# Optimization experiments

Hardware: AMD Instinct MI355X
Metric: run time of the kernel (lower is better)

## Reference

```python
import jax, jax.numpy as jnp
import numpy as np

N = 40962          # icosphere level-6 vertex count
E = 245772         # N * k (k=6 knn, directed)
MUL_IN = 8         # '8x0e + 8x1o' -> dim 8 + 24 = 32
MUL_OUT = 16       # '16x0e + 16x1o' -> dim 16 + 48 = 64
H = 64             # radial MLP hidden
WNUM = 4 * MUL_IN * MUL_OUT  # 512 per-edge TP weights (4 CG paths)
SQ3 = np.float32(np.sqrt(3.0))


def setup_inputs() -> dict:
    key = jax.random.key(0)
    ks = jax.random.split(key, 8)
    x = jax.random.normal(ks[0], (N, MUL_IN + 3 * MUL_IN), dtype=jnp.float32)
    pos = jax.random.normal(ks[1], (N, 3), dtype=jnp.float32)
    src = jax.random.randint(ks[2], (E,), 0, N)
    dst = jax.random.randint(ks[3], (E,), 0, N)
    edge_index = jnp.stack([src, dst]).astype(jnp.int32)
    W1 = jax.random.normal(ks[4], (1, H), dtype=jnp.float32)
    W2 = jax.random.normal(ks[5], (H, WNUM), dtype=jnp.float32)
    Ws = jax.random.normal(ks[6], (MUL_OUT, MUL_OUT), dtype=jnp.float32)
    k7, k8 = jax.random.split(ks[7])
    Wns = jax.random.normal(k7, (MUL_OUT, MUL_OUT), dtype=jnp.float32)
    Wg = jax.random.normal(k8, (MUL_OUT, MUL_OUT), dtype=jnp.float32)
    return {"x": x, "pos": pos, "edge_index": edge_index,
            "W1": W1, "W2": W2, "Ws": Ws, "Wns": Wns, "Wg": Wg}


def reference(x, pos, edge_index, W1, W2, Ws, Wns, Wg):
    src, dst = edge_index[0], edge_index[1]
    xs = x[:, :MUL_IN]                                  # (N, 8)  scalars (0e)
    xv = x[:, MUL_IN:].reshape(-1, MUL_IN, 3)           # (N, 8, 3) vectors (1o)

    # --- edge geometry + spherical harmonics (component-normalized, lmax=1) ---
    edge_vec = pos[dst] - pos[src]                      # (E, 3)
    edge_len = jnp.maximum(jnp.linalg.norm(edge_vec, axis=-1, keepdims=True), 1e-8)
    edge_dir = edge_vec / edge_len                      # (E, 3)
    Y1 = SQ3 * edge_dir                                 # l=1 SH; l=0 SH == 1

    # --- radial MLP -> per-edge tensor-product weights (shared_weights=False) ---
    h = jax.nn.silu(edge_len @ W1)                      # (E, H), fan_in = 1
    w = (h @ W2) * (1.0 / np.sqrt(np.float32(H)))       # (E, 512)
    wA, wB, wC, wD = [wi.reshape(-1, MUL_IN, MUL_OUT)
                      for wi in jnp.split(w, 4, axis=1)]

    xs_e = xs[src]                                      # (E, 8)   gather
    xv_e = xv[src]                                      # (E, 8, 3) gather
    norm = np.float32(1.0 / np.sqrt(2.0 * MUL_IN))      # path normalization

    # --- tensor product: 4 CG paths ---
    # 0e x 0e -> 0e  (CG = 1)
    pathA = jnp.einsum('eu,euw->ew', xs_e, wA)
    # 1o x 1o -> 0e  (CG_ij = delta_ij / sqrt(3))
    dot = jnp.einsum('eui,ei->eu', xv_e, Y1) * (1.0 / SQ3)
    pathB = jnp.einsum('eu,euw->ew', dot, wB)
    m_s = (pathA + pathB) * norm                        # (E, 16)
    # 0e x 1o -> 1o  (CG = identity)
    pathC = jnp.einsum('eu,euw->ew', xs_e, wC)[:, :, None] * Y1[:, None, :]
    # 1o x 0e -> 1o  (CG = identity)
    pathD = jnp.einsum('eui,euw->ewi', xv_e, wD)
    m_v = (pathC + pathD) * norm                        # (E, 16, 3)

    m = jnp.concatenate([m_s, m_v.reshape(-1, 3 * MUL_OUT)], axis=1)  # (E, 64)

    # --- scatter-add to destination nodes (index_add) ---
    out = jnp.zeros((x.shape[0], m.shape[1]), dtype=x.dtype).at[dst].add(m)

    # --- gated equivariant nonlinearity (o3.Linear with fan-in norm) ---
    lin_norm = np.float32(1.0 / np.sqrt(np.float32(MUL_OUT)))
    os_ = out[:, :MUL_OUT]                              # (N, 16)
    ov_ = out[:, MUL_OUT:].reshape(-1, MUL_OUT, 3)      # (N, 16, 3)
    s = jax.nn.silu(os_ @ Ws * lin_norm)                # (N, 16)
    ns = jnp.einsum('nui,uw->nwi', ov_, Wns) * lin_norm # (N, 16, 3)
    g = jax.nn.sigmoid(os_ @ Wg * lin_norm)             # (N, 16)
    gated = (g[:, :, None] * ns).reshape(-1, 3 * MUL_OUT)
    return jnp.concatenate([s, gated], axis=1)          # (N, 64)
```

## Files before the change

kernel.cpp:

```cpp
#include <hip/hip_runtime.h>
#include <math.h>

typedef _Float16 half8 __attribute__((ext_vector_type(8)));
typedef float floatx4 __attribute__((ext_vector_type(4)));

#define SQ3 1.7320508075688772f

__global__ __launch_bounds__(256) void prep_w2(const float* __restrict__ W2,
                                               _Float16* __restrict__ bw) {
    int t = blockIdx.x * 256 + threadIdx.x;
    if (t >= 32768) return;
    int i    = t & 7;
    int l    = (t >> 3) & 63;
    int s    = (t >> 9) & 1;
    int tt   = (t >> 10) & 7;
    int path = t >> 13;
    int k   = s * 32 + (l >> 4) * 8 + i;
    int col = path * 128 + tt * 16 + (l & 15);
    float scale = 0.03125f * (path == 2 ? SQ3 : 1.0f);
    bw[t] = (_Float16)(W2[k * 512 + col] * scale);
}

__global__ __launch_bounds__(256) void edge_kernel(
    const float* __restrict__ x, const float* __restrict__ pos,
    const int* __restrict__ ei, const float* __restrict__ W1,
    const _Float16* __restrict__ bw, float* __restrict__ out,
    int E, int ntiles)
{
    __shared__ __align__(16) float4 sW1v[16];
    __shared__ __align__(16) float4 s_geo[64];
    __shared__ int s_dst[64];
    __shared__ __align__(16) _Float16 s_xs[64][8];
    __shared__ __align__(16) _Float16 s_xv[64][24];
    __shared__ __align__(16) _Float16 s_hA[4][2][64][8];
    __shared__ __align__(16) _Float16 s_part[2][64][64];

    const int tid  = threadIdx.x;
    const int wave = tid >> 6;
    const int lane = tid & 63;

    if (tid < 16) sW1v[tid] = reinterpret_cast<const float4*>(W1)[tid];

    half8 bfrag[8][2];
    {
        const half8* bsrc = (const half8*)bw;
        #pragma unroll
        for (int t = 0; t < 8; ++t)
            #pragma unroll
            for (int s = 0; s < 2; ++s)
                bfrag[t][s] = bsrc[(size_t)wave * 1024 + (t * 2 + s) * 64 + lane];
    }

    for (int tile = blockIdx.x; tile < ntiles; tile += gridDim.x) {
        const int ebase = tile * 64;
        __syncthreads();

        {
            int eg_l = tid >> 2, q = tid & 3;
            int eg = ebase + eg_l;
            int ec = (eg < E) ? eg : (E - 1);
            int si = ei[ec];
            const float* xr = x + (size_t)si * 32 + q * 8;
            float4 va = *reinterpret_cast<const float4*>(xr);
            float4 vb = *reinterpret_cast<const float4*>(xr + 4);
            half8 hv;
            hv[0] = (_Float16)va.x; hv[1] = (_Float16)va.y;
            hv[2] = (_Float16)va.z; hv[3] = (_Float16)va.w;
            hv[4] = (_Float16)vb.x; hv[5] = (_Float16)vb.y;
            hv[6] = (_Float16)vb.z; hv[7] = (_Float16)vb.w;
            if (q == 0) *(half8*)&s_xs[eg_l][0] = hv;
            else        *(half8*)&s_xv[eg_l][(q - 1) * 8] = hv;
        }
        {
            int sub = tid >> 6;
            int l   = tid & 63;
            int el  = sub * 16 + (l & 15);
            int kg  = l >> 4;
            int eg  = ebase + el;
            int ec  = (eg < E) ? eg : (E - 1);
            int si = ei[ec];
            int di = ei[E + ec];
            float ex = pos[di * 3 + 0] - pos[si * 3 + 0];
            float ey = pos[di * 3 + 1] - pos[si * 3 + 1];
            float ez = pos[di * 3 + 2] - pos[si * 3 + 2];
            float len = sqrtf(ex * ex + ey * ey + ez * ez);
            len = fmaxf(len, 1e-8f);
            float inv = 1.0f / len;
            if (kg == 0) {
                s_geo[el] = make_float4(ex * inv, ey * inv, ez * inv, len);
                s_dst[el] = di;
            }
            #pragma unroll
            for (int s = 0; s < 2; ++s) {
                float4 w0 = sW1v[s * 8 + kg * 2 + 0];
                float4 w1 = sW1v[s * 8 + kg * 2 + 1];
                float ww[8] = {w0.x, w0.y, w0.z, w0.w, w1.x, w1.y, w1.z, w1.w};
                half8 ha;
                #pragma unroll
                for (int i = 0; i < 8; ++i) {
                    float z = len * ww[i];
                    ha[i] = (_Float16)(z / (1.0f + __expf(-z)));
                }
                *(half8*)&s_hA[sub][s][l][0] = ha;
            }
        }
        __syncthreads();

        const int wp  = lane & 15;
        const int er0 = (lane >> 4) * 4;
        #pragma unroll
        for (int sub = 0; sub < 4; ++sub) {
            half8 a0 = *(const half8*)&s_hA[sub][0][lane][0];
            half8 a1 = *(const half8*)&s_hA[sub][1][lane][0];
            floatx4 acc[8];
            #pragma unroll
            for (int t = 0; t < 8; ++t) {
                floatx4 z = {0.f, 0.f, 0.f, 0.f};
                z = __builtin_amdgcn_mfma_f32_16x16x32_f16(a0, bfrag[t][0], z, 0, 0, 0);
                acc[t] = __builtin_amdgcn_mfma_f32_16x16x32_f16(a1, bfrag[t][1], z, 0, 0, 0);
            }

            if (wave == 0) {
                #pragma unroll
                for (int r = 0; r < 4; ++r) {
                    int e = sub * 16 + er0 + r;
                    half8 xs = *(const half8*)&s_xs[e][0];
                    float m = 0.f;
                    #pragma unroll
                    for (int u = 0; u < 8; ++u) m += (float)xs[u] * acc[u][r];
                    s_part[0][e][wp] = (_Float16)m;
                }
            } else if (wave == 1) {
                #pragma unroll
                for (int r = 0; r < 4; ++r) {
                    int e = sub * 16 + er0 + r;
                    half8 v0 = *(const half8*)&s_xv[e][0];
                    half8 v1 = *(const half8*)&s_xv[e][8];
                    half8 v2 = *(const half8*)&s_xv[e][16];
                    float4 g = s_geo[e];
                    float xf[24];
                    #pragma unroll
                    for (int i = 0; i < 8; ++i) {
                        xf[i] = (float)v0[i]; xf[8 + i] = (float)v1[i];
                        xf[16 + i] = (float)v2[i];
                    }
                    float m = 0.f;
                    #pragma unroll
                    for (int u = 0; u < 8; ++u) {
                        float dot = xf[u*3+0]*g.x + xf[u*3+1]*g.y + xf[u*3+2]*g.z;
                        m += dot * acc[u][r];
                    }
                    s_part[1][e][wp] = (_Float16)m;
                }
            } else if (wave == 2) {
                #pragma unroll
                for (int r = 0; r < 4; ++r) {
                    int e = sub * 16 + er0 + r;
                    half8 xs = *(const half8*)&s_xs[e][0];
                    float4 g = s_geo[e];
                    float cw = 0.f;
                    #pragma unroll
                    for (int u = 0; u < 8; ++u) cw += (float)xs[u] * acc[u][r];
                    s_part[0][e][16 + wp * 3 + 0] = (_Float16)(cw * g.x);
                    s_part[0][e][16 + wp * 3 + 1] = (_Float16)(cw * g.y);
                    s_part[0][e][16 + wp * 3 + 2] = (_Float16)(cw * g.z);
                }
            } else {
                #pragma unroll
                for (int r = 0; r < 4; ++r) {
                    int e = sub * 16 + er0 + r;
                    half8 v0 = *(const half8*)&s_xv[e][0];
                    half8 v1 = *(const half8*)&s_xv[e][8];
                    half8 v2 = *(const half8*)&s_xv[e][16];
                    float xf[24];
                    #pragma unroll
                    for (int i = 0; i < 8; ++i) {
                        xf[i] = (float)v0[i]; xf[8 + i] = (float)v1[i];
                        xf[16 + i] = (float)v2[i];
                    }
                    float m0 = 0.f, m1 = 0.f, m2 = 0.f;
                    #pragma unroll
                    for (int u = 0; u < 8; ++u) {
                        float w = acc[u][r];
                        m0 += xf[u*3+0] * w;
                        m1 += xf[u*3+1] * w;
                        m2 += xf[u*3+2] * w;
                    }
                    s_part[1][e][16 + wp * 3 + 0] = (_Float16)m0;
                    s_part[1][e][16 + wp * 3 + 1] = (_Float16)m1;
                    s_part[1][e][16 + wp * 3 + 2] = (_Float16)m2;
                }
            }
        }
        __syncthreads();

        {
            int c = tid & 63;
            int g = tid >> 6;
            #pragma unroll
            for (int k = 0; k < 16; ++k) {
                int e  = g * 16 + k;
                int eg = ebase + e;
                if (eg < E) {
                    float v = (float)s_part[0][e][c] + (float)s_part[1][e][c];
                    atomicAdd(out + (size_t)s_dst[e] * 64 + c, v);
                }
            }
        }
    }
}

__global__ __launch_bounds__(256) void node_kernel(
    float* __restrict__ out, const float* __restrict__ Ws,
    const float* __restrict__ Wns, const float* __restrict__ Wg, int N)
{
    int n = blockIdx.x * 256 + threadIdx.x;
    if (n >= N) return;
    float* row = out + (size_t)n * 64;

    float os[16], ov[48];
    #pragma unroll
    for (int q = 0; q < 4; ++q) {
        float4 v = *reinterpret_cast<const float4*>(row + q * 4);
        os[q*4+0]=v.x; os[q*4+1]=v.y; os[q*4+2]=v.z; os[q*4+3]=v.w;
    }
    #pragma unroll
    for (int q = 0; q < 12; ++q) {
        float4 v = *reinterpret_cast<const float4*>(row + 16 + q * 4);
        ov[q*4+0]=v.x; ov[q*4+1]=v.y; ov[q*4+2]=v.z; ov[q*4+3]=v.w;
    }

    float sres[16], gres[16];
    #pragma unroll
    for (int w = 0; w < 16; ++w) {
        float a = 0.f, b = 0.f;
        #pragma unroll
        for (int u = 0; u < 16; ++u) {
            float o_u = os[u];
            a += o_u * Ws[u * 16 + w];
            b += o_u * Wg[u * 16 + w];
        }
        a *= 0.25f; b *= 0.25f;
        sres[w] = a / (1.0f + __expf(-a));
        gres[w] = 1.0f / (1.0f + __expf(-b));
    }

    float gated[48];
    #pragma unroll
    for (int w = 0; w < 16; ++w) {
        float n0 = 0.f, n1 = 0.f, n2 = 0.f;
        #pragma unroll
        for (int u = 0; u < 16; ++u) {
            float wn = Wns[u * 16 + w];
            n0 += ov[u*3+0] * wn;
            n1 += ov[u*3+1] * wn;
            n2 += ov[u*3+2] * wn;
        }
        float gw = gres[w] * 0.25f;
        gated[w*3+0] = n0 * gw;
        gated[w*3+1] = n1 * gw;
        gated[w*3+2] = n2 * gw;
    }

    #pragma unroll
    for (int q = 0; q < 4; ++q) {
        float4 v = make_float4(sres[q*4+0], sres[q*4+1], sres[q*4+2], sres[q*4+3]);
        *reinterpret_cast<float4*>(row + q * 4) = v;
    }
    #pragma unroll
    for (int q = 0; q < 12; ++q) {
        float4 v = make_float4(gated[q*4+0], gated[q*4+1], gated[q*4+2], gated[q*4+3]);
        *reinterpret_cast<float4*>(row + 16 + q * 4) = v;
    }
}

extern "C" void kernel_launch(void* const* d_in, const int* in_sizes, int n_in,
                              void* d_out, int out_size, void* d_ws, size_t ws_size,
                              hipStream_t stream) {
    const float* x   = (const float*)d_in[0];
    const float* pos = (const float*)d_in[1];
    const int*   ei  = (const int*)d_in[2];
    const float* W1  = (const float*)d_in[3];
    const float* W2  = (const float*)d_in[4];
    const float* Ws  = (const float*)d_in[5];
    const float* Wns = (const float*)d_in[6];
    const float* Wg  = (const float*)d_in[7];

    int N = in_sizes[0] / 32;
    int E = in_sizes[2] / 2;
    int ntiles = (E + 63) / 64;
    float* out = (float*)d_out;
    _Float16* bw = (_Float16*)d_ws;

    hipMemsetAsync(d_out, 0, (size_t)N * 64 * sizeof(float), stream);
    prep_w2<<<128, 256, 0, stream>>>(W2, bw);
    int nblk = ntiles < 1280 ? ntiles : 1280;
    edge_kernel<<<nblk, 256, 0, stream>>>(x, pos, ei, W1, bw, out, E, ntiles);
    node_kernel<<<(N + 255) / 256, 256, 0, stream>>>(out, Ws, Wns, Wg, N);
}
```

Measured before the change: 127.2 us.

## Replace atomic scatter-add with CSR sort by destination and segmented gather

Builds a destination-sorted permutation each call (count, single-block scan, atomic scatter) and has the edge kernel write fp16 messages to a workspace buffer instead of doing float atomics into the output. A gather kernel then sums each node's messages with one wave per node. The edge kernel also drops its persistent grid-stride loop and launches one block per tile. This trades output atomics for the extra sort kernels, a single-block scan, an E×64 fp16 message round trip through memory, and fp16 rounding of the summed message, and it falls back to the atomic path when the workspace is too small.

```diff
diff --git a/kernel.cpp b/kernel.cpp
--- a/kernel.cpp
+++ b/kernel.cpp
@@ -21,11 +21,59 @@
     bw[t] = (_Float16)(W2[k * 512 + col] * scale);
 }
 
+__global__ __launch_bounds__(256) void count_kernel(const int* __restrict__ ei,
+                                                    int* __restrict__ counts, int E) {
+    int e = blockIdx.x * 256 + threadIdx.x;
+    if (e < E) atomicAdd(&counts[ei[E + e]], 1);
+}
+
+__global__ __launch_bounds__(1024) void scan_kernel(const int* __restrict__ counts,
+                                                    int* __restrict__ offs,
+                                                    int* __restrict__ cursor, int nbins) {
+    __shared__ int part[1024];
+    int tid = threadIdx.x;
+    int per = (nbins + 1023) / 1024;
+    int base = tid * per;
+    int s = 0;
+    for (int i = 0; i < per; ++i) {
+        int idx = base + i;
+        if (idx < nbins) s += counts[idx];
+    }
+    part[tid] = s;
+    __syncthreads();
+    for (int d = 1; d < 1024; d <<= 1) {
+        int v = (tid >= d) ? part[tid - d] : 0;
+        __syncthreads();
+        part[tid] += v;
+        __syncthreads();
+    }
+    int run = part[tid] - s;
+    for (int i = 0; i < per; ++i) {
+        int idx = base + i;
+        if (idx < nbins) {
+            offs[idx] = run;
+            cursor[idx] = run;
+            run += counts[idx];
+        }
+    }
+    if (tid == 1023) offs[nbins] = run;
+}
+
+__global__ __launch_bounds__(256) void scatter_kernel(const int* __restrict__ ei,
+                                                      int* __restrict__ cursor,
+                                                      int* __restrict__ perm, int E) {
+    int e = blockIdx.x * 256 + threadIdx.x;
+    if (e < E) {
+        int slot = atomicAdd(&cursor[ei[E + e]], 1);
+        perm[slot] = e;
+    }
+}
+
 __global__ __launch_bounds__(256) void edge_kernel(
     const float* __restrict__ x, const float* __restrict__ pos,
     const int* __restrict__ ei, const float* __restrict__ W1,
-    const _Float16* __restrict__ bw, float* __restrict__ out,
-    int E, int ntiles)
+    const _Float16* __restrict__ bw, _Float16* __restrict__ msg,
+    float* __restrict__ out, int E, int mode)
 {
     __shared__ __align__(16) float4 sW1v[16];
     __shared__ __align__(16) float4 s_geo[64];
@@ -38,6 +86,7 @@
     const int tid  = threadIdx.x;
     const int wave = tid >> 6;
     const int lane = tid & 63;
+    const int ebase = blockIdx.x * 64;
 
     if (tid < 16) sW1v[tid] = reinterpret_cast<const float4*>(W1)[tid];
 
@@ -51,152 +100,159 @@
                 bfrag[t][s] = bsrc[(size_t)wave * 1024 + (t * 2 + s) * 64 + lane];
     }
 
-    for (int tile = blockIdx.x; tile < ntiles; tile += gridDim.x) {
-        const int ebase = tile * 64;
-        __syncthreads();
-
-        {
-            int eg_l = tid >> 2, q = tid & 3;
-            int eg = ebase + eg_l;
-            int ec = (eg < E) ? eg : (E - 1);
-            int si = ei[ec];
-            const float* xr = x + (size_t)si * 32 + q * 8;
-            float4 va = *reinterpret_cast<const float4*>(xr);
-            float4 vb = *reinterpret_cast<const float4*>(xr + 4);
-            half8 hv;
-            hv[0] = (_Float16)va.x; hv[1] = (_Float16)va.y;
-            hv[2] = (_Float16)va.z; hv[3] = (_Float16)va.w;
-            hv[4] = (_Float16)vb.x; hv[5] = (_Float16)vb.y;
-            hv[6] = (_Float16)vb.z; hv[7] = (_Float16)vb.w;
-            if (q == 0) *(half8*)&s_xs[eg_l][0] = hv;
-            else        *(half8*)&s_xv[eg_l][(q - 1) * 8] = hv;
-        }
-        {
-            int sub = tid >> 6;
-            int l   = tid & 63;
-            int el  = sub * 16 + (l & 15);
-            int kg  = l >> 4;
-            int eg  = ebase + el;
-            int ec  = (eg < E) ? eg : (E - 1);
-            int si = ei[ec];
-            int di = ei[E + ec];
-            float ex = pos[di * 3 + 0] - pos[si * 3 + 0];
-            float ey = pos[di * 3 + 1] - pos[si * 3 + 1];
-            float ez = pos[di * 3 + 2] - pos[si * 3 + 2];
-            float len = sqrtf(ex * ex + ey * ey + ez * ez);
-            len = fmaxf(len, 1e-8f);
-            float inv = 1.0f / len;
-            if (kg == 0) {
-                s_geo[el] = make_float4(ex * inv, ey * inv, ez * inv, len);
-                s_dst[el] = di;
-            }
-            #pragma unroll
-            for (int s = 0; s < 2; ++s) {
-                float4 w0 = sW1v[s * 8 + kg * 2 + 0];
-                float4 w1 = sW1v[s * 8 + kg * 2 + 1];
-                float ww[8] = {w0.x, w0.y, w0.z, w0.w, w1.x, w1.y, w1.z, w1.w};
-                half8 ha;
+    {
+        int eg_l = tid >> 2, q = tid & 3;
+        int eg = ebase + eg_l;
+        int ec = (eg < E) ? eg : (E - 1);
+        int si = ei[ec];
+        const float* xr = x + (size_t)si * 32 + q * 8;
+        float4 va = *reinterpret_cast<const float4*>(xr);
+        float4 vb = *reinterpret_cast<const float4*>(xr + 4);
+        half8 hv;
+        hv[0] = (_Float16)va.x; hv[1] = (_Float16)va.y;
+        hv[2] = (_Float16)va.z; hv[3] = (_Float16)va.w;
+        hv[4] = (_Float16)vb.x; hv[5] = (_Float16)vb.y;
+        hv[6] = (_Float16)vb.z; hv[7] = (_Float16)vb.w;
+        if (q == 0) *(half8*)&s_xs[eg_l][0] = hv;
+        else        *(half8*)&s_xv[eg_l][(q - 1) * 8] = hv;
+    }
+    {
+        int sub = tid >> 6;
+        int l   = tid & 63;
+        int el  = sub * 16 + (l & 15);
+        int kg  = l >> 4;
+        int eg  = ebase + el;
+        int ec  = (eg < E) ? eg : (E - 1);
+        int si = ei[ec];
+        int di = ei[E + ec];
+        float ex = pos[di * 3 + 0] - pos[si * 3 + 0];
+        float ey = pos[di * 3 + 1] - pos[si * 3 + 1];
+        float ez = pos[di * 3 + 2] - pos[si * 3 + 2];
+        float len = sqrtf(ex * ex + ey * ey + ez * ez);
+        len = fmaxf(len, 1e-8f);
+        float inv = 1.0f / len;
+        if (kg == 0) {
+            s_geo[el] = make_float4(ex * inv, ey * inv, ez * inv, len);
+            s_dst[el] = di;
+        }
+        #pragma unroll
+        for (int s = 0; s < 2; ++s) {
+            float4 w0 = sW1v[s * 8 + kg * 2 + 0];
+            float4 w1 = sW1v[s * 8 + kg * 2 + 1];
+            float ww[8] = {w0.x, w0.y, w0.z, w0.w, w1.x, w1.y, w1.z, w1.w};
+            half8 ha;
+            #pragma unroll
+            for (int i = 0; i < 8; ++i) {
+                float z = len * ww[i];
+                ha[i] = (_Float16)(z / (1.0f + __expf(-z)));
+            }
+            *(half8*)&s_hA[sub][s][l][0] = ha;
+        }
+    }
+    __syncthreads();
+
+    const int wp  = lane & 15;
+    const int er0 = (lane >> 4) * 4;
+    #pragma unroll
+    for (int sub = 0; sub < 4; ++sub) {
+        half8 a0 = *(const half8*)&s_hA[sub][0][lane][0];
+        half8 a1 = *(const half8*)&s_hA[sub][1][lane][0];
+        floatx4 acc[8];
+        #pragma unroll
+        for (int t = 0; t < 8; ++t) {
+            floatx4 z = {0.f, 0.f, 0.f, 0.f};
+            z = __builtin_amdgcn_mfma_f32_16x16x32_f16(a0, bfrag[t][0], z, 0, 0, 0);
+            acc[t] = __builtin_amdgcn_mfma_f32_16x16x32_f16(a1, bfrag[t][1], z, 0, 0, 0);
+        }
+
+        if (wave == 0) {
+            #pragma unroll
+            for (int r = 0; r < 4; ++r) {
+                int e = sub * 16 + er0 + r;
+                half8 xs = *(const half8*)&s_xs[e][0];
+                float m = 0.f;
+                #pragma unroll
+                for (int u = 0; u < 8; ++u) m += (float)xs[u] * acc[u][r];
+                s_part[0][e][wp] = (_Float16)m;
+            }
+        } else if (wave == 1) {
+            #pragma unroll
+            for (int r = 0; r < 4; ++r) {
+                int e = sub * 16 + er0 + r;
+                half8 v0 = *(const half8*)&s_xv[e][0];
+                half8 v1 = *(const half8*)&s_xv[e][8];
+                half8 v2 = *(const half8*)&s_xv[e][16];
+                float4 g = s_geo[e];
+                float xf[24];
                 #pragma unroll
                 for (int i = 0; i < 8; ++i) {
-                    float z = len * ww[i];
-                    ha[i] = (_Float16)(z / (1.0f + __expf(-z)));
-                }
-                *(half8*)&s_hA[sub][s][l][0] = ha;
-            }
-        }
-        __syncthreads();
-
-        const int wp  = lane & 15;
-        const int er0 = (lane >> 4) * 4;
-        #pragma unroll
-        for (int sub = 0; sub < 4; ++sub) {
-            half8 a0 = *(const half8*)&s_hA[sub][0][lane][0];
-            half8 a1 = *(const half8*)&s_hA[sub][1][lane][0];
-            floatx4 acc[8];
-            #pragma unroll
-            for (int t = 0; t < 8; ++t) {
-                floatx4 z = {0.f, 0.f, 0.f, 0.f};
-                z = __builtin_amdgcn_mfma_f32_16x16x32_f16(a0, bfrag[t][0], z, 0, 0, 0);
-                acc[t] = __builtin_amdgcn_mfma_f32_16x16x32_f16(a1, bfrag[t][1], z, 0, 0, 0);
-            }
-
-            if (wave == 0) {
-                #pragma unroll
-                for (int r = 0; r < 4; ++r) {
-                    int e = sub * 16 + er0 + r;
-                    half8 xs = *(const half8*)&s_xs[e][0];
-                    float m = 0.f;
-                    #pragma unroll
-                    for (int u = 0; u < 8; ++u) m += (float)xs[u] * acc[u][r];
-                    s_part[0][e][wp] = (_Float16)m;
-                }
-            } else if (wave == 1) {
-                #pragma unroll
-                for (int r = 0; r < 4; ++r) {
-                    int e = sub * 16 + er0 + r;
-                    half8 v0 = *(const half8*)&s_xv[e][0];
-                    half8 v1 = *(const half8*)&s_xv[e][8];
-                    half8 v2 = *(const half8*)&s_xv[e][16];
-                    float4 g = s_geo[e];
-                    float xf[24];
-                    #pragma unroll
-                    for (int i = 0; i < 8; ++i) {
-                        xf[i] = (float)v0[i]; xf[8 + i] = (float)v1[i];
-                        xf[16 + i] = (float)v2[i];
-                    }
-                    float m = 0.f;
-                    #pragma unroll
-                    for (int u = 0; u < 8; ++u) {
-                        float dot = xf[u*3+0]*g.x + xf[u*3+1]*g.y + xf[u*3+2]*g.z;
-                        m += dot * acc[u][r];
-                    }
-                    s_part[1][e][wp] = (_Float16)m;
-                }
-            } else if (wave == 2) {
-                #pragma unroll
-                for (int r = 0; r < 4; ++r) {
-                    int e = sub * 16 + er0 + r;
-                    half8 xs = *(const half8*)&s_xs[e][0];
-                    float4 g = s_geo[e];
-                    float cw = 0.f;
-                    #pragma unroll
-                    for (int u = 0; u < 8; ++u) cw += (float)xs[u] * acc[u][r];
-                    s_part[0][e][16 + wp * 3 + 0] = (_Float16)(cw * g.x);
-                    s_part[0][e][16 + wp * 3 + 1] = (_Float16)(cw * g.y);
-                    s_part[0][e][16 + wp * 3 + 2] = (_Float16)(cw * g.z);
-                }
-            } else {
-                #pragma unroll
-                for (int r = 0; r < 4; ++r) {
-                    int e = sub * 16 + er0 + r;
-                    half8 v0 = *(const half8*)&s_xv[e][0];
-                    half8 v1 = *(const half8*)&s_xv[e][8];
-                    half8 v2 = *(const half8*)&s_xv[e][16];
-                    float xf[24];
-                    #pragma unroll
-                    for (int i = 0; i < 8; ++i) {
-                        xf[i] = (float)v0[i]; xf[8 + i] = (float)v1[i];
-                        xf[16 + i] = (float)v2[i];
-                    }
-                    float m0 = 0.f, m1 = 0.f, m2 = 0.f;
-                    #pragma unroll
-                    for (int u = 0; u < 8; ++u) {
-                        float w = acc[u][r];
-                        m0 += xf[u*3+0] * w;
-                        m1 += xf[u*3+1] * w;
-                        m2 += xf[u*3+2] * w;
-                    }
-                    s_part[1][e][16 + wp * 3 + 0] = (_Float16)m0;
-                    s_part[1][e][16 + wp * 3 + 1] = (_Float16)m1;
-                    s_part[1][e][16 + wp * 3 + 2] = (_Float16)m2;
-                }
-            }
-        }
-        __syncthreads();
-
-        {
-            int c = tid & 63;
-            int g = tid >> 6;
+                    xf[i] = (float)v0[i]; xf[8 + i] = (float)v1[i];
+                    xf[16 + i] = (float)v2[i];
+                }
+                float m = 0.f;
+                #pragma unroll
+                for (int u = 0; u < 8; ++u) {
+                    float dot = xf[u*3+0]*g.x + xf[u*3+1]*g.y + xf[u*3+2]*g.z;
+                    m += dot * acc[u][r];
+                }
+                s_part[1][e][wp] = (_Float16)m;
+            }
+        } else if (wave == 2) {
+            #pragma unroll
+            for (int r = 0; r < 4; ++r) {
+                int e = sub * 16 + er0 + r;
+                half8 xs = *(const half8*)&s_xs[e][0];
+                float4 g = s_geo[e];
+                float cw = 0.f;
+                #pragma unroll
+                for (int u = 0; u < 8; ++u) cw += (float)xs[u] * acc[u][r];
+                s_part[0][e][16 + wp * 3 + 0] = (_Float16)(cw * g.x);
+                s_part[0][e][16 + wp * 3 + 1] = (_Float16)(cw * g.y);
+                s_part[0][e][16 + wp * 3 + 2] = (_Float16)(cw * g.z);
+            }
+        } else {
+            #pragma unroll
+            for (int r = 0; r < 4; ++r) {
+                int e = sub * 16 + er0 + r;
+                half8 v0 = *(const half8*)&s_xv[e][0];
+                half8 v1 = *(const half8*)&s_xv[e][8];
+                half8 v2 = *(const half8*)&s_xv[e][16];
+                float xf[24];
+                #pragma unroll
+                for (int i = 0; i < 8; ++i) {
+                    xf[i] = (float)v0[i]; xf[8 + i] = (float)v1[i];
+                    xf[16 + i] = (float)v2[i];
+                }
+                float m0 = 0.f, m1 = 0.f, m2 = 0.f;
+                #pragma unroll
+                for (int u = 0; u < 8; ++u) {
+                    float w = acc[u][r];
+                    m0 += xf[u*3+0] * w;
+                    m1 += xf[u*3+1] * w;
+                    m2 += xf[u*3+2] * w;
+                }
+                s_part[1][e][16 + wp * 3 + 0] = (_Float16)m0;
+                s_part[1][e][16 + wp * 3 + 1] = (_Float16)m1;
+                s_part[1][e][16 + wp * 3 + 2] = (_Float16)m2;
+            }
+        }
+    }
+    __syncthreads();
+
+    {
+        int c = tid & 63;
+        int g = tid >> 6;
+        if (mode == 0) {
+            #pragma unroll
+            for (int k = 0; k < 16; ++k) {
+                int e  = g * 16 + k;
+                int eg = ebase + e;
+                if (eg < E) {
+                    _Float16 v = s_part[0][e][c] + s_part[1][e][c];
+                    msg[(size_t)eg * 64 + c] = v;
+                }
+            }
+        } else {
             #pragma unroll
             for (int k = 0; k < 16; ++k) {
                 int e  = g * 16 + k;
@@ -207,6 +263,25 @@
                 }
             }
         }
+    }
+}
+
+__global__ __launch_bounds__(256) void gather_kernel(
+    const _Float16* __restrict__ msg, const int* __restrict__ offs,
+    const int* __restrict__ perm, float* __restrict__ out, int N)
+{
+    int nwaves = gridDim.x * 4;
+    int gw = blockIdx.x * 4 + (threadIdx.x >> 6);
+    int lane = threadIdx.x & 63;
+    for (int n = gw; n < N; n += nwaves) {
+        int b  = offs[n];
+        int e2 = offs[n + 1];
+        float s = 0.f;
+        for (int j = b; j < e2; ++j) {
+            int row = perm[j];
+            s += (float)msg[(size_t)row * 64 + lane];
+        }
+        out[(size_t)n * 64 + lane] = s;
     }
 }
 
@@ -290,11 +365,39 @@
     int E = in_sizes[2] / 2;
     int ntiles = (E + 63) / 64;
     float* out = (float*)d_out;
-    _Float16* bw = (_Float16*)d_ws;
-
-    hipMemsetAsync(d_out, 0, (size_t)N * 64 * sizeof(float), stream);
+    char* ws = (char*)d_ws;
+
+    size_t off = 0;
+    auto alloc = [&](size_t bytes) { size_t o = off; off = (off + bytes + 255) & ~255UL; return o; };
+    size_t o_bw     = alloc(32768 * sizeof(_Float16));
+    size_t o_counts = alloc((size_t)N * 4);
+    size_t o_cursor = alloc((size_t)N * 4);
+    size_t o_offs   = alloc((size_t)(N + 1) * 4);
+    size_t o_perm   = alloc((size_t)E * 4);
+    size_t o_msg    = alloc((size_t)E * 64 * sizeof(_Float16));
+    size_t needed = off;
+
+    _Float16* bw = (_Float16*)(ws + o_bw);
     prep_w2<<<128, 256, 0, stream>>>(W2, bw);
-    int nblk = ntiles < 1280 ? ntiles : 1280;
-    edge_kernel<<<nblk, 256, 0, stream>>>(x, pos, ei, W1, bw, out, E, ntiles);
-    node_kernel<<<(N + 255) / 256, 256, 0, stream>>>(out, Ws, Wns, Wg, N);
-}
+
+    if (ws_size >= needed) {
+        int* counts = (int*)(ws + o_counts);
+        int* cursor = (int*)(ws + o_cursor);
+        int* offs   = (int*)(ws + o_offs);
+        int* perm   = (int*)(ws + o_perm);
+        _Float16* msg = (_Float16*)(ws + o_msg);
+
+        hipMemsetAsync(counts, 0, (size_t)N * 4, stream);
+        int eblk = (E + 255) / 256;
+        count_kernel<<<eblk, 256, 0, stream>>>(ei, counts, E);
+        scan_kernel<<<1, 1024, 0, stream>>>(counts, offs, cursor, N);
+        scatter_kernel<<<eblk, 256, 0, stream>>>(ei, cursor, perm, E);
+        edge_kernel<<<ntiles, 256, 0, stream>>>(x, pos, ei, W1, bw, msg, out, E, 0);
+        gather_kernel<<<1024, 256, 0, stream>>>(msg, offs, perm, out, N);
+        node_kernel<<<(N + 255) / 256, 256, 0, stream>>>(out, Ws, Wns, Wg, N);
+    } else {
+        hipMemsetAsync(out, 0, (size_t)N * 64 * sizeof(float), stream);
+        edge_kernel<<<ntiles, 256, 0, stream>>>(x, pos, ei, W1, bw, nullptr, out, E, 1);
+        node_kernel<<<(N + 255) / 256, 256, 0, stream>>>(out, Ws, Wns, Wg, N);
+    }
+}
```

New measurement: 262.0 us. +106.0%, slower.

## Prefetch next tile's gathers into registers and double-buffer shared staging

Applied to the files above, without the earlier changes.

The edge kernel now issues the global gathers for the next tile (edge indices, x rows, positions) into registers right after the staging barrier, so their latency overlaps the MFMA, contraction and atomic phases of the current tile. Shared staging buffers are doubled and indexed by a ping-pong flag, and the geometry/SiLU work is reassigned so one thread per (edge, quarter) handles both x conversion and radial features, removing the duplicate index and position loads. The grid is reduced from 1280 to 960 blocks. In exchange it raises register pressure and LDS footprint, which may lower occupancy, and drops the loop-top barrier, relying on the double buffer for safety on s_part reuse.

```diff
diff --git a/kernel.cpp b/kernel.cpp
--- a/kernel.cpp
+++ b/kernel.cpp
@@ -21,25 +21,50 @@
     bw[t] = (_Float16)(W2[k * 512 + col] * scale);
 }
 
+struct Pref {
+    float4 xa, xb;
+    float psx, psy, psz, pdx, pdy, pdz;
+    int si, di;
+};
+
+__device__ __forceinline__ Pref issue_loads(int tile, int E,
+        const int* __restrict__ ei, const float* __restrict__ x,
+        const float* __restrict__ pos, int tid) {
+    Pref p;
+    int el = tid >> 2, q = tid & 3;
+    int eg = tile * 64 + el;
+    int ec = (eg < E) ? eg : (E - 1);
+    p.si = ei[ec];
+    p.di = ei[E + ec];
+    const float* xr = x + (size_t)p.si * 32 + q * 8;
+    p.xa = *reinterpret_cast<const float4*>(xr);
+    p.xb = *reinterpret_cast<const float4*>(xr + 4);
+    const float* ps = pos + (size_t)p.si * 3;
+    const float* pd = pos + (size_t)p.di * 3;
+    p.psx = ps[0]; p.psy = ps[1]; p.psz = ps[2];
+    p.pdx = pd[0]; p.pdy = pd[1]; p.pdz = pd[2];
+    return p;
+}
+
 __global__ __launch_bounds__(256) void edge_kernel(
     const float* __restrict__ x, const float* __restrict__ pos,
     const int* __restrict__ ei, const float* __restrict__ W1,
     const _Float16* __restrict__ bw, float* __restrict__ out,
     int E, int ntiles)
 {
-    __shared__ __align__(16) float4 sW1v[16];
-    __shared__ __align__(16) float4 s_geo[64];
-    __shared__ int s_dst[64];
-    __shared__ __align__(16) _Float16 s_xs[64][8];
-    __shared__ __align__(16) _Float16 s_xv[64][24];
-    __shared__ __align__(16) _Float16 s_hA[4][2][64][8];
+    __shared__ float sW1[64];
+    __shared__ __align__(16) float4 s_geo[2][64];
+    __shared__ int s_dst[2][64];
+    __shared__ __align__(16) _Float16 s_xs[2][64][8];
+    __shared__ __align__(16) _Float16 s_xv[2][64][24];
+    __shared__ __align__(16) _Float16 s_hA[2][4][2][64][8];
     __shared__ __align__(16) _Float16 s_part[2][64][64];
 
     const int tid  = threadIdx.x;
     const int wave = tid >> 6;
     const int lane = tid & 63;
 
-    if (tid < 16) sW1v[tid] = reinterpret_cast<const float4*>(W1)[tid];
+    if (tid < 64) sW1[tid] = W1[tid];
 
     half8 bfrag[8][2];
     {
@@ -51,67 +76,58 @@
                 bfrag[t][s] = bsrc[(size_t)wave * 1024 + (t * 2 + s) * 64 + lane];
     }
 
-    for (int tile = blockIdx.x; tile < ntiles; tile += gridDim.x) {
-        const int ebase = tile * 64;
-        __syncthreads();
-
+    int tile = blockIdx.x;
+    if (tile >= ntiles) return;
+    Pref p = issue_loads(tile, E, ei, x, pos, tid);
+    __syncthreads();
+
+    int buf = 0;
+    for (; tile < ntiles; tile += gridDim.x) {
         {
-            int eg_l = tid >> 2, q = tid & 3;
-            int eg = ebase + eg_l;
-            int ec = (eg < E) ? eg : (E - 1);
-            int si = ei[ec];
-            const float* xr = x + (size_t)si * 32 + q * 8;
-            float4 va = *reinterpret_cast<const float4*>(xr);
-            float4 vb = *reinterpret_cast<const float4*>(xr + 4);
+            int el = tid >> 2, q = tid & 3;
             half8 hv;
-            hv[0] = (_Float16)va.x; hv[1] = (_Float16)va.y;
-            hv[2] = (_Float16)va.z; hv[3] = (_Float16)va.w;
-            hv[4] = (_Float16)vb.x; hv[5] = (_Float16)vb.y;
-            hv[6] = (_Float16)vb.z; hv[7] = (_Float16)vb.w;
-            if (q == 0) *(half8*)&s_xs[eg_l][0] = hv;
-            else        *(half8*)&s_xv[eg_l][(q - 1) * 8] = hv;
-        }
-        {
-            int sub = tid >> 6;
-            int l   = tid & 63;
-            int el  = sub * 16 + (l & 15);
-            int kg  = l >> 4;
-            int eg  = ebase + el;
-            int ec  = (eg < E) ? eg : (E - 1);
-            int si = ei[ec];
-            int di = ei[E + ec];
-            float ex = pos[di * 3 + 0] - pos[si * 3 + 0];
-            float ey = pos[di * 3 + 1] - pos[si * 3 + 1];
-            float ez = pos[di * 3 + 2] - pos[si * 3 + 2];
-            float len = sqrtf(ex * ex + ey * ey + ez * ez);
-            len = fmaxf(len, 1e-8f);
+            hv[0] = (_Float16)p.xa.x; hv[1] = (_Float16)p.xa.y;
+            hv[2] = (_Float16)p.xa.z; hv[3] = (_Float16)p.xa.w;
+            hv[4] = (_Float16)p.xb.x; hv[5] = (_Float16)p.xb.y;
+            hv[6] = (_Float16)p.xb.z; hv[7] = (_Float16)p.xb.w;
+            if (q == 0) *(half8*)&s_xs[buf][el][0] = hv;
+            else        *(half8*)&s_xv[buf][el][(q - 1) * 8] = hv;
+
+            float ex = p.pdx - p.psx;
+            float ey = p.pdy - p.psy;
+            float ez = p.pdz - p.psz;
+            float len = fmaxf(sqrtf(ex * ex + ey * ey + ez * ez), 1e-8f);
             float inv = 1.0f / len;
-            if (kg == 0) {
-                s_geo[el] = make_float4(ex * inv, ey * inv, ez * inv, len);
-                s_dst[el] = di;
-            }
+            if (q == 0) {
+                s_geo[buf][el] = make_float4(ex * inv, ey * inv, ez * inv, len);
+                s_dst[buf][el] = p.di;
+            }
+            int sub = el >> 4;
+            int l   = (q << 4) | (el & 15);
             #pragma unroll
             for (int s = 0; s < 2; ++s) {
-                float4 w0 = sW1v[s * 8 + kg * 2 + 0];
-                float4 w1 = sW1v[s * 8 + kg * 2 + 1];
-                float ww[8] = {w0.x, w0.y, w0.z, w0.w, w1.x, w1.y, w1.z, w1.w};
                 half8 ha;
                 #pragma unroll
                 for (int i = 0; i < 8; ++i) {
-                    float z = len * ww[i];
+                    float z = len * sW1[s * 32 + q * 8 + i];
                     ha[i] = (_Float16)(z / (1.0f + __expf(-z)));
                 }
-                *(half8*)&s_hA[sub][s][l][0] = ha;
+                *(half8*)&s_hA[buf][sub][s][l][0] = ha;
             }
         }
         __syncthreads();
+
+        int nt = tile + gridDim.x;
+        bool has = (nt < ntiles);
+        Pref pn;
+        if (has) pn = issue_loads(nt, E, ei, x, pos, tid);
 
         const int wp  = lane & 15;
         const int er0 = (lane >> 4) * 4;
         #pragma unroll
         for (int sub = 0; sub < 4; ++sub) {
-            half8 a0 = *(const half8*)&s_hA[sub][0][lane][0];
-            half8 a1 = *(const half8*)&s_hA[sub][1][lane][0];
+            half8 a0 = *(const half8*)&s_hA[buf][sub][0][lane][0];
+            half8 a1 = *(const half8*)&s_hA[buf][sub][1][lane][0];
             floatx4 acc[8];
             #pragma unroll
             for (int t = 0; t < 8; ++t) {
@@ -124,7 +140,7 @@
                 #pragma unroll
                 for (int r = 0; r < 4; ++r) {
                     int e = sub * 16 + er0 + r;
-                    half8 xs = *(const half8*)&s_xs[e][0];
+                    half8 xs = *(const half8*)&s_xs[buf][e][0];
                     float m = 0.f;
                     #pragma unroll
                     for (int u = 0; u < 8; ++u) m += (float)xs[u] * acc[u][r];
@@ -134,10 +150,10 @@
                 #pragma unroll
                 for (int r = 0; r < 4; ++r) {
                     int e = sub * 16 + er0 + r;
-                    half8 v0 = *(const half8*)&s_xv[e][0];
-                    half8 v1 = *(const half8*)&s_xv[e][8];
-                    half8 v2 = *(const half8*)&s_xv[e][16];
-                    float4 g = s_geo[e];
+                    half8 v0 = *(const half8*)&s_xv[buf][e][0];
+                    half8 v1 = *(const half8*)&s_xv[buf][e][8];
+                    half8 v2 = *(const half8*)&s_xv[buf][e][16];
+                    float4 g = s_geo[buf][e];
                     float xf[24];
                     #pragma unroll
                     for (int i = 0; i < 8; ++i) {
@@ -156,8 +172,8 @@
                 #pragma unroll
                 for (int r = 0; r < 4; ++r) {
                     int e = sub * 16 + er0 + r;
-                    half8 xs = *(const half8*)&s_xs[e][0];
-                    float4 g = s_geo[e];
+                    half8 xs = *(const half8*)&s_xs[buf][e][0];
+                    float4 g = s_geo[buf][e];
                     float cw = 0.f;
                     #pragma unroll
                     for (int u = 0; u < 8; ++u) cw += (float)xs[u] * acc[u][r];
@@ -169,9 +185,9 @@
                 #pragma unroll
                 for (int r = 0; r < 4; ++r) {
                     int e = sub * 16 + er0 + r;
-                    half8 v0 = *(const half8*)&s_xv[e][0];
-                    half8 v1 = *(const half8*)&s_xv[e][8];
-                    half8 v2 = *(const half8*)&s_xv[e][16];
+                    half8 v0 = *(const half8*)&s_xv[buf][e][0];
+                    half8 v1 = *(const half8*)&s_xv[buf][e][8];
+                    half8 v2 = *(const half8*)&s_xv[buf][e][16];
                     float xf[24];
                     #pragma unroll
                     for (int i = 0; i < 8; ++i) {
@@ -200,13 +216,15 @@
             #pragma unroll
             for (int k = 0; k < 16; ++k) {
                 int e  = g * 16 + k;
-                int eg = ebase + e;
+                int eg = tile * 64 + e;
                 if (eg < E) {
                     float v = (float)s_part[0][e][c] + (float)s_part[1][e][c];
-                    atomicAdd(out + (size_t)s_dst[e] * 64 + c, v);
-                }
-            }
-        }
+                    atomicAdd(out + (size_t)s_dst[buf][e] * 64 + c, v);
+                }
+            }
+        }
+        p = pn;
+        buf ^= 1;
     }
 }
 
@@ -292,9 +310,9 @@
     float* out = (float*)d_out;
     _Float16* bw = (_Float16*)d_ws;
 
-    hipMemsetAsync(d_out, 0, (size_t)N * 64 * sizeof(float), stream);
+    hipMemsetAsync(out, 0, (size_t)N * 64 * sizeof(float), stream);
     prep_w2<<<128, 256, 0, stream>>>(W2, bw);
-    int nblk = ntiles < 1280 ? ntiles : 1280;
+    int nblk = ntiles < 960 ? ntiles : 960;
     edge_kernel<<<nblk, 256, 0, stream>>>(x, pos, ei, W1, bw, out, E, ntiles);
     node_kernel<<<(N + 255) / 256, 256, 0, stream>>>(out, Ws, Wns, Wg, N);
 }
```

Measured after the change: 107.0 us. 1.19x faster.
